# Kernel tuning notes

Hardware: AMD Instinct MI355X
Metric: run time of the kernel (lower is better)

The kernel has to match this reference:

```python
import jax, jax.numpy as jnp
import numpy as np

B, T, D, H, K = 8, 4096, 768, 12, 64
EPS_WKV = 1e-9
EPS_GN = 1e-5


def setup_inputs() -> dict:
    key = jax.random.key(0)
    ks = jax.random.split(key, 12)
    x = jax.random.normal(ks[0], (B, T, D), jnp.float32)
    # linear projection weights (torch nn.Linear stores [out, in]; y = x @ W.T)
    W_r = jax.random.normal(ks[1], (D, D), jnp.float32) * 0.02
    W_k = jax.random.normal(ks[2], (D, D), jnp.float32) * 0.02
    W_v = jax.random.normal(ks[3], (D, D), jnp.float32) * 0.02
    W_o = jax.random.normal(ks[4], (D, D), jnp.float32) * 0.02
    time_mix_r = jax.random.uniform(ks[5], (D,), jnp.float32)
    time_mix_k = jax.random.uniform(ks[6], (D,), jnp.float32)
    time_mix_v = jax.random.uniform(ks[7], (D,), jnp.float32)
    # around the module's init values (time_decay ~ -0.075, time_first ~ 0.15 at layer 6/12)
    time_decay = -0.075 + 0.1 * jax.random.normal(ks[8], (H, K), jnp.float32)
    time_first = 0.15 + 0.1 * jax.random.normal(ks[9], (H, K), jnp.float32)
    gn_weight = jnp.ones((D,), jnp.float32)
    gn_bias = jnp.zeros((D,), jnp.float32)
    return {
        "x": x,
        "time_mix_r": time_mix_r, "time_mix_k": time_mix_k, "time_mix_v": time_mix_v,
        "time_decay": time_decay, "time_first": time_first,
        "W_r": W_r, "W_k": W_k, "W_v": W_v, "W_o": W_o,
        "gn_weight": gn_weight, "gn_bias": gn_bias,
    }


def reference(x, time_mix_r, time_mix_k, time_mix_v, time_decay, time_first,
              W_r, W_k, W_v, W_o, gn_weight, gn_bias):
    Bx, Tx, Dx = x.shape
    Hx, Kx = time_decay.shape
    # token-shift: previous timestep (zero-initialized state)
    x_prev = jnp.concatenate([jnp.zeros_like(x[:, :1]), x[:, :-1]], axis=1)
    xr = x * time_mix_r + x_prev * (1.0 - time_mix_r)
    xk = x * time_mix_k + x_prev * (1.0 - time_mix_k)
    xv = x * time_mix_v + x_prev * (1.0 - time_mix_v)
    r = jax.nn.sigmoid(xr @ W_r.T).reshape(Bx, Tx, Hx, Kx)
    k = (xk @ W_k.T).reshape(Bx, Tx, Hx, Kx)
    v = (xv @ W_v.T).reshape(Bx, Tx, Hx, Kx)

    w = jnp.exp(-jnp.exp(time_decay))   # [H,K] decay per channel
    eu = jnp.exp(time_first)            # [H,K] bonus for current token

    def step(carry, kv_t):
        num, den = carry                # each [B,H,K]
        k_t, v_t = kv_t                 # each [B,H,K]
        ek = jnp.exp(k_t)
        wkv = (num + eu * ek * v_t) / (den + eu * ek + EPS_WKV)
        return (num * w + ek * v_t, den * w + ek), wkv

    k_tm = jnp.moveaxis(k, 1, 0)        # [T,B,H,K]
    v_tm = jnp.moveaxis(v, 1, 0)
    init = (jnp.zeros((Bx, Hx, Kx), x.dtype), jnp.zeros((Bx, Hx, Kx), x.dtype))
    _, wkv = jax.lax.scan(step, init, (k_tm, v_tm))
    out = jnp.moveaxis(wkv, 0, 1)       # [B,T,H,K]

    y = r * out                         # [B,T,H,K]
    # torch GroupNorm(H, D) on [B, D, T]: normalize each group over (K channels x T steps)
    mean = y.mean(axis=(1, 3), keepdims=True)
    var = y.var(axis=(1, 3), keepdims=True)
    y = (y - mean) * jax.lax.rsqrt(var + EPS_GN)
    y = y * gn_weight.reshape(1, 1, Hx, Kx) + gn_bias.reshape(1, 1, Hx, Kx)
    return y.reshape(Bx, Tx, Dx) @ W_o.T
```

## Files before the change

### kernel.cpp

```cpp
#include <hip/hip_runtime.h>
#include <hip/hip_bf16.h>
#include <cstdint>

#define B_ 8
#define T_ 4096
#define D_ 768
#define H_ 12
#define M_ (B_*T_)
#define CHUNKS 256
#define CLEN 16
#define WELEM (D_*D_)
#define NCH (B_*H_*64)

typedef __attribute__((ext_vector_type(8))) short bf16x8;
typedef __attribute__((ext_vector_type(4))) float f32x4;

static __device__ __forceinline__ unsigned short f2bf(float f) {
  __hip_bfloat16 h = __float2bfloat16(f);
  return __builtin_bit_cast(unsigned short, h);
}
static __device__ __forceinline__ float bf2f(unsigned short u) {
  unsigned v = ((unsigned)u) << 16;
  return __builtin_bit_cast(float, v);
}

static __device__ __forceinline__ void async16(const void* g, void* l) {
  __builtin_amdgcn_global_load_lds(
      (const __attribute__((address_space(1))) unsigned int*)g,
      (__attribute__((address_space(3))) unsigned int*)l, 16, 0, 0);
}

__global__ __launch_bounds__(256) void zero_out_kernel(float* __restrict__ out, size_t n4) {
  size_t gid = (size_t)blockIdx.x * 256 + threadIdx.x;
  if (gid < n4) *(float4*)(out + gid * 4) = make_float4(0.f, 0.f, 0.f, 0.f);
}

__global__ __launch_bounds__(256) void mix_kernel(
    const float* __restrict__ x, const float* __restrict__ tmr,
    const float* __restrict__ tmk, const float* __restrict__ tmv,
    unsigned short* __restrict__ xr, unsigned short* __restrict__ xk,
    unsigned short* __restrict__ xv) {
  size_t gid = (size_t)blockIdx.x * 256 + threadIdx.x;
  size_t idx4 = gid * 4;
  int d = (int)(idx4 % D_);
  size_t row = idx4 / D_;
  int t = (int)(row & (T_ - 1));
  float4 xc = *(const float4*)(x + idx4);
  float4 xp = make_float4(0.f, 0.f, 0.f, 0.f);
  if (t > 0) xp = *(const float4*)(x + idx4 - D_);
  float4 mr = *(const float4*)(tmr + d);
  float4 mk = *(const float4*)(tmk + d);
  float4 mv = *(const float4*)(tmv + d);
  ushort4 orr, okk, ovv;
  orr.x = f2bf(xc.x*mr.x + xp.x*(1.f-mr.x));
  orr.y = f2bf(xc.y*mr.y + xp.y*(1.f-mr.y));
  orr.z = f2bf(xc.z*mr.z + xp.z*(1.f-mr.z));
  orr.w = f2bf(xc.w*mr.w + xp.w*(1.f-mr.w));
  okk.x = f2bf(xc.x*mk.x + xp.x*(1.f-mk.x));
  okk.y = f2bf(xc.y*mk.y + xp.y*(1.f-mk.y));
  okk.z = f2bf(xc.z*mk.z + xp.z*(1.f-mk.z));
  okk.w = f2bf(xc.w*mk.w + xp.w*(1.f-mk.w));
  ovv.x = f2bf(xc.x*mv.x + xp.x*(1.f-mv.x));
  ovv.y = f2bf(xc.y*mv.y + xp.y*(1.f-mv.y));
  ovv.z = f2bf(xc.z*mv.z + xp.z*(1.f-mv.z));
  ovv.w = f2bf(xc.w*mv.w + xp.w*(1.f-mv.w));
  *(ushort4*)(xr + idx4) = orr;
  *(ushort4*)(xk + idx4) = okk;
  *(ushort4*)(xv + idx4) = ovv;
}

__global__ __launch_bounds__(256) void wconv_kernel(
    const float* __restrict__ a, const float* __restrict__ b,
    const float* __restrict__ c, const float* __restrict__ d,
    unsigned short* __restrict__ o) {
  size_t gid = (size_t)blockIdx.x * 256 + threadIdx.x;
  size_t idx4 = gid * 4;
  size_t mi = idx4 / WELEM;
  size_t off = idx4 % WELEM;
  const float* src = (mi == 0) ? a : (mi == 1) ? b : (mi == 2) ? c : d;
  float4 v = *(const float4*)(src + off);
  ushort4 u;
  u.x = f2bf(v.x); u.y = f2bf(v.y); u.z = f2bf(v.z); u.w = f2bf(v.w);
  *(ushort4*)(o + idx4) = u;
}

template<int ACT, int OBF>
__global__ __launch_bounds__(256) void gemm_nt(
    const unsigned short* __restrict__ A,
    const unsigned short* __restrict__ Bw,
    void* __restrict__ Cv, int M, int N, int Kd) {
  __shared__ __align__(16) unsigned short smem[4][128 * 64];
  const int tid = threadIdx.x;
  const int wave = tid >> 6, lane = tid & 63;
  const int quad = lane >> 4, l16 = lane & 15;

  int nwg = gridDim.x * gridDim.y;
  int lin = blockIdx.y * gridDim.x + blockIdx.x;
  int q = nwg >> 3, r = nwg & 7;
  int xcd = lin & 7, off = lin >> 3;
  int swz = (xcd < r ? xcd * (q + 1) : r * (q + 1) + (xcd - r) * q) + off;
  const int m0 = (swz / gridDim.x) * 128;
  const int n0 = (swz % gridDim.x) * 128;
  const int wm = (wave & 1) * 64, wn = (wave >> 1) * 64;

  auto stage = [&](int buf, int kb) {
    unsigned short* As = smem[buf];
    unsigned short* Bs = smem[buf] + 128 * 32;
#pragma unroll
    for (int j = 0; j < 2; ++j) {
      int chunk = j * 256 + tid;
      int row = chunk >> 2, slot = chunk & 3;
      int ks = slot ^ ((row >> 1) & 3);
      async16(A  + ((size_t)(m0 + row) * Kd + kb + ks * 8), &As[chunk * 8]);
      async16(Bw + ((size_t)(n0 + row) * Kd + kb + ks * 8), &Bs[chunk * 8]);
    }
  };

  f32x4 acc[4][4] = {};
  const int NT = Kd >> 5;

  stage(0, 0); stage(1, 32); stage(2, 64);
  for (int t = 0; t < NT; ++t) {
    if (t < NT - 2)       asm volatile("s_waitcnt vmcnt(8)" ::: "memory");
    else if (t == NT - 2) asm volatile("s_waitcnt vmcnt(4)" ::: "memory");
    else                  asm volatile("s_waitcnt vmcnt(0)" ::: "memory");
    __builtin_amdgcn_s_barrier();
    if (t + 3 < NT) stage((t + 3) & 3, (t + 3) * 32);
    const unsigned short* As = smem[t & 3];
    const unsigned short* Bs = smem[t & 3] + 128 * 32;
    bf16x8 a[4], b[4];
#pragma unroll
    for (int i = 0; i < 4; ++i) {
      int ra = wm + i * 16 + l16;
      a[i] = *(const bf16x8*)&As[ra * 32 + ((quad ^ ((ra >> 1) & 3)) * 8)];
      int rb = wn + i * 16 + l16;
      b[i] = *(const bf16x8*)&Bs[rb * 32 + ((quad ^ ((rb >> 1) & 3)) * 8)];
    }
#pragma unroll
    for (int i = 0; i < 4; ++i)
#pragma unroll
      for (int jj = 0; jj < 4; ++jj)
        acc[i][jj] = __builtin_amdgcn_mfma_f32_16x16x32_bf16(a[i], b[jj], acc[i][jj], 0, 0, 0);
  }

  if (OBF) {
    unsigned short* Cs = (unsigned short*)smem;
#pragma unroll
    for (int i = 0; i < 4; ++i) {
#pragma unroll
      for (int jj = 0; jj < 4; ++jj) {
        int col = wn + jj * 16 + l16;
#pragma unroll
        for (int rr = 0; rr < 4; ++rr) {
          int row = wm + i * 16 + quad * 4 + rr;
          float v = acc[i][jj][rr];
          if (ACT == 1) v = 1.f / (1.f + __expf(-v));
          int cg = (col >> 3) ^ (row & 7);
          Cs[row * 128 + cg * 8 + (col & 7)] = f2bf(v);
        }
      }
    }
    __syncthreads();
#pragma unroll
    for (int g = 0; g < 8; ++g) {
      int gi = g * 256 + tid;
      int row = gi >> 4, cg = gi & 15;
      int sg = cg ^ (row & 7);
      bf16x8 vv = *(const bf16x8*)&Cs[row * 128 + sg * 8];
      *(bf16x8*)((unsigned short*)Cv + (size_t)(m0 + row) * N + n0 + cg * 8) = vv;
    }
  } else {
#pragma unroll
    for (int i = 0; i < 4; ++i) {
      int rowb = m0 + wm + i * 16 + quad * 4;
#pragma unroll
      for (int jj = 0; jj < 4; ++jj) {
        int col = n0 + wn + jj * 16 + l16;
#pragma unroll
        for (int rr = 0; rr < 4; ++rr) {
          float v = acc[i][jj][rr];
          ((float*)Cv)[(size_t)(rowb + rr) * N + col] = v;
        }
      }
    }
  }
}

__global__ __launch_bounds__(256) void wkv_pass1(
    const unsigned short* __restrict__ Kb, const unsigned short* __restrict__ Vb,
    const float* __restrict__ td,
    float* __restrict__ sumN, float* __restrict__ sumD) {
  int gid = blockIdx.x * 256 + threadIdx.x;
  int kg = gid & 7;
  int tmp = gid >> 3;
  int h = tmp % H_;
  tmp /= H_;
  int b = tmp % B_;
  int c = tmp / B_;
  const float* tdp = td + h * 64 + kg * 8;
  float w[8], num[8], den[8];
#pragma unroll
  for (int j = 0; j < 8; ++j) {
    w[j] = __expf(-__expf(tdp[j]));
    num[j] = 0.f; den[j] = 0.f;
  }
  size_t base = ((size_t)(b * T_ + c * CLEN)) * D_ + h * 64 + kg * 8;
#pragma unroll 4
  for (int i = 0; i < CLEN; ++i) {
    bf16x8 k8 = *(const bf16x8*)(Kb + base + (size_t)i * D_);
    bf16x8 v8 = *(const bf16x8*)(Vb + base + (size_t)i * D_);
#pragma unroll
    for (int j = 0; j < 8; ++j) {
      float ek = __expf(bf2f((unsigned short)k8[j]));
      num[j] = num[j] * w[j] + ek * bf2f((unsigned short)v8[j]);
      den[j] = den[j] * w[j] + ek;
    }
  }
  int ob = ((c * B_ + b) * H_ + h) * 64 + kg * 8;
  *(float4*)(sumN + ob)     = make_float4(num[0], num[1], num[2], num[3]);
  *(float4*)(sumN + ob + 4) = make_float4(num[4], num[5], num[6], num[7]);
  *(float4*)(sumD + ob)     = make_float4(den[0], den[1], den[2], den[3]);
  *(float4*)(sumD + ob + 4) = make_float4(den[4], den[5], den[6], den[7]);
}

__global__ __launch_bounds__(256) void wkv_pass2(
    const float* __restrict__ sumN, const float* __restrict__ sumD,
    const float* __restrict__ td,
    float* __restrict__ prefN, float* __restrict__ prefD,
    float* __restrict__ gstats) {
  __shared__ float tile[256][64];
  int bid = blockIdx.x;
  if (bid == 0 && threadIdx.x < 192) gstats[threadIdx.x] = 0.f;
  int bh = bid >> 1, qd = bid & 1;
  const float* src = qd ? sumD : sumN;
  float* dst = qd ? prefD : prefN;
  int h = bh % H_;
  int base = bh * 64;
  int t = threadIdx.x;
  {
    int c4 = (t & 15) * 4;
    int rg = t >> 4;
#pragma unroll 4
    for (int i = 0; i < 16; ++i) {
      int row = rg * 16 + i;
      *(float4*)&tile[row][c4] = *(const float4*)&src[(size_t)row * NCH + base + c4];
    }
  }
  __syncthreads();
  int ch = t & 63, g = t >> 6;
  float w = __expf(-__expf(td[h * 64 + ch]));
  float wL = w;
#pragma unroll
  for (int i = 0; i < 4; ++i) wL *= wL;
  float v = 0.f;
  for (int i = 0; i < 64; ++i) {
    int row = g * 64 + i;
    v = v * wL + tile[row][ch];
    tile[row][ch] = v;
  }
  __syncthreads();
  float wL64 = wL;
#pragma unroll
  for (int i = 0; i < 6; ++i) wL64 *= wL64;
  float E = 0.f;
  for (int gp = 0; gp < g; ++gp)
    E = E * wL64 + tile[gp * 64 + 63][ch];
  float f = 1.f;
  for (int i = 0; i < 64; ++i) {
    int row = g * 64 + i;
    float P = (i == 0) ? E : tile[row - 1][ch] + E * f;
    dst[(size_t)row * NCH + base + ch] = P;
    f *= wL;
  }
}

__global__ __launch_bounds__(256) void wkv_pass3(
    const unsigned short* __restrict__ Kb, const unsigned short* __restrict__ Vb,
    unsigned short* __restrict__ RY,
    const float* __restrict__ td, const float* __restrict__ tf,
    const float* __restrict__ prefN, const float* __restrict__ prefD,
    float* __restrict__ gsum, float* __restrict__ gsq) {
  int gid = blockIdx.x * 256 + threadIdx.x;
  int kg = gid & 7;
  int tmp = gid >> 3;
  int h = tmp % H_;
  tmp /= H_;
  int b = tmp % B_;
  int c = tmp / B_;
  const float* tdp = td + h * 64 + kg * 8;
  const float* tfp = tf + h * 64 + kg * 8;
  float w[8], eu[8], num[8], den[8];
  int sb = ((c * B_ + b) * H_ + h) * 64 + kg * 8;
  float4 n0 = *(const float4*)(prefN + sb), n1 = *(const float4*)(prefN + sb + 4);
  float4 d0 = *(const float4*)(prefD + sb), d1 = *(const float4*)(prefD + sb + 4);
  num[0]=n0.x; num[1]=n0.y; num[2]=n0.z; num[3]=n0.w;
  num[4]=n1.x; num[5]=n1.y; num[6]=n1.z; num[7]=n1.w;
  den[0]=d0.x; den[1]=d0.y; den[2]=d0.z; den[3]=d0.w;
  den[4]=d1.x; den[5]=d1.y; den[6]=d1.z; den[7]=d1.w;
#pragma unroll
  for (int j = 0; j < 8; ++j) {
    w[j]  = __expf(-__expf(tdp[j]));
    eu[j] = __expf(tfp[j]);
  }
  size_t base = ((size_t)(b * T_ + c * CLEN)) * D_ + h * 64 + kg * 8;
  float s1 = 0.f, s2 = 0.f;
#pragma unroll 4
  for (int i = 0; i < CLEN; ++i) {
    size_t idx = base + (size_t)i * D_;
    bf16x8 k8 = *(const bf16x8*)(Kb + idx);
    bf16x8 v8 = *(const bf16x8*)(Vb + idx);
    bf16x8 r8 = *(const bf16x8*)(RY + idx);
    bf16x8 y8;
#pragma unroll
    for (int j = 0; j < 8; ++j) {
      float kk = bf2f((unsigned short)k8[j]);
      float vv = bf2f((unsigned short)v8[j]);
      float rr = bf2f((unsigned short)r8[j]);
      float ek = __expf(kk);
      float wkv = __fdividef(num[j] + eu[j] * ek * vv, den[j] + eu[j] * ek + 1e-9f);
      unsigned short ybf = f2bf(rr * wkv);
      y8[j] = (short)ybf;
      float y = bf2f(ybf);
      s1 += y; s2 += y * y;
      num[j] = num[j] * w[j] + ek * vv;
      den[j] = den[j] * w[j] + ek;
    }
    *(bf16x8*)(RY + idx) = y8;
  }
#pragma unroll
  for (int off = 4; off; off >>= 1) {
    s1 += __shfl_xor(s1, off);
    s2 += __shfl_xor(s2, off);
  }
  if (kg == 0) {
    atomicAdd(&gsum[b * H_ + h], s1);
    atomicAdd(&gsq [b * H_ + h], s2);
  }
}

__global__ __launch_bounds__(256) void gn_kernel(
    const unsigned short* __restrict__ Y, const float* __restrict__ gsum,
    const float* __restrict__ gsq, const float* __restrict__ gw,
    const float* __restrict__ gb, unsigned short* __restrict__ Ybf) {
  size_t gid = (size_t)blockIdx.x * 256 + threadIdx.x;
  size_t idx4 = gid * 4;
  int d = (int)(idx4 % D_);
  size_t row = idx4 / D_;
  int b = (int)(row >> 12);
  int h = d >> 6;
  int g = b * H_ + h;
  const float inv = 1.f / (float)(T_ * 64);
  float mean = gsum[g] * inv;
  float var = gsq[g] * inv - mean * mean;
  float rstd = rsqrtf(var + 1e-5f);
  ushort4 yu = *(const ushort4*)(Y + idx4);
  float4 wv = *(const float4*)(gw + d);
  float4 bv = *(const float4*)(gb + d);
  ushort4 o;
  o.x = f2bf((bf2f(yu.x) - mean) * rstd * wv.x + bv.x);
  o.y = f2bf((bf2f(yu.y) - mean) * rstd * wv.y + bv.y);
  o.z = f2bf((bf2f(yu.z) - mean) * rstd * wv.z + bv.z);
  o.w = f2bf((bf2f(yu.w) - mean) * rstd * wv.w + bv.w);
  *(ushort4*)(Ybf + idx4) = o;
}

extern "C" void kernel_launch(void* const* d_in, const int* in_sizes, int n_in,
                              void* d_out, int out_size, void* d_ws, size_t ws_size,
                              hipStream_t stream) {
  (void)in_sizes; (void)n_in;
  const float* x   = (const float*)d_in[0];
  const float* tmr = (const float*)d_in[1];
  const float* tmk = (const float*)d_in[2];
  const float* tmv = (const float*)d_in[3];
  const float* td  = (const float*)d_in[4];
  const float* tf  = (const float*)d_in[5];
  const float* Wr  = (const float*)d_in[6];
  const float* Wk  = (const float*)d_in[7];
  const float* Wv  = (const float*)d_in[8];
  const float* Wo  = (const float*)d_in[9];
  const float* gw  = (const float*)d_in[10];
  const float* gb  = (const float*)d_in[11];
  float* out = (float*)d_out;

  constexpr size_t MD = (size_t)M_ * D_;
  constexpr size_t NEED = 4 * (MD * 2)
                        + (size_t)4 * WELEM * 2
                        + 4 * ((size_t)CHUNKS * NCH * 4)
                        + 1024;
  if (ws_size < NEED) {
    zero_out_kernel<<<(int)((MD / 4 + 255) / 256), 256, 0, stream>>>(out, MD / 4);
    return;
  }

  char* ws = (char*)d_ws;
  unsigned short* XR = (unsigned short*)ws; ws += MD * 2;
  unsigned short* XK = (unsigned short*)ws; ws += MD * 2;
  unsigned short* XV = (unsigned short*)ws; ws += MD * 2;
  unsigned short* Rb = (unsigned short*)ws; ws += MD * 2;
  unsigned short* Wb = (unsigned short*)ws; ws += (size_t)4 * WELEM * 2;
  float* sumN  = (float*)ws; ws += (size_t)CHUNKS * NCH * 4;
  float* sumD  = (float*)ws; ws += (size_t)CHUNKS * NCH * 4;
  float* prefN = (float*)ws; ws += (size_t)CHUNKS * NCH * 4;
  float* prefD = (float*)ws; ws += (size_t)CHUNKS * NCH * 4;
  float* gstats = (float*)ws; ws += 1024;
  unsigned short* Kb = XR;
  unsigned short* Vb = XK;
  unsigned short* Yb = XV;

  mix_kernel<<<(int)(MD / 1024), 256, 0, stream>>>(x, tmr, tmk, tmv, XR, XK, XV);
  wconv_kernel<<<(4 * WELEM / 4) / 256, 256, 0, stream>>>(Wr, Wk, Wv, Wo, Wb);

  dim3 ggrid(D_ / 128, M_ / 128);
  gemm_nt<1, 1><<<ggrid, 256, 0, stream>>>(XR, Wb,             Rb, M_, D_, D_);
  gemm_nt<0, 1><<<ggrid, 256, 0, stream>>>(XK, Wb + WELEM,     Kb, M_, D_, D_);
  gemm_nt<0, 1><<<ggrid, 256, 0, stream>>>(XV, Wb + 2 * WELEM, Vb, M_, D_, D_);

  wkv_pass1<<<(CHUNKS * NCH / 8) / 256, 256, 0, stream>>>(Kb, Vb, td, sumN, sumD);
  wkv_pass2<<<192, 256, 0, stream>>>(sumN, sumD, td, prefN, prefD, gstats);
  wkv_pass3<<<(CHUNKS * NCH / 8) / 256, 256, 0, stream>>>(Kb, Vb, Rb, td, tf,
                                                          prefN, prefD, gstats, gstats + 96);
  gn_kernel<<<(int)(MD / 1024), 256, 0, stream>>>(Rb, gstats, gstats + 96, gw, gb, Yb);

  gemm_nt<0, 0><<<ggrid, 256, 0, stream>>>(Yb, Wb + 3 * WELEM, out, M_, D_, D_);
}
```

Measured before the change: 538.6 us.

## Fold GroupNorm into per-batch output weights and bias, drop gn pass

Result: faster. 515.8 us (-4.2%).

```diff
diff --git a/kernel.cpp b/kernel.cpp
--- a/kernel.cpp
+++ b/kernel.cpp
@@ -71,25 +71,24 @@
 
 __global__ __launch_bounds__(256) void wconv_kernel(
     const float* __restrict__ a, const float* __restrict__ b,
-    const float* __restrict__ c, const float* __restrict__ d,
-    unsigned short* __restrict__ o) {
+    const float* __restrict__ c, unsigned short* __restrict__ o) {
   size_t gid = (size_t)blockIdx.x * 256 + threadIdx.x;
   size_t idx4 = gid * 4;
   size_t mi = idx4 / WELEM;
   size_t off = idx4 % WELEM;
-  const float* src = (mi == 0) ? a : (mi == 1) ? b : (mi == 2) ? c : d;
+  const float* src = (mi == 0) ? a : (mi == 1) ? b : c;
   float4 v = *(const float4*)(src + off);
   ushort4 u;
   u.x = f2bf(v.x); u.y = f2bf(v.y); u.z = f2bf(v.z); u.w = f2bf(v.w);
   *(ushort4*)(o + idx4) = u;
 }
 
-template<int ACT, int OBF>
-__global__ __launch_bounds__(256) void gemm_nt(
+template<int ACT, int OBF, int BIAS>
+__global__ __launch_bounds__(256, 3) void gemm_nt(
     const unsigned short* __restrict__ A,
     const unsigned short* __restrict__ Bw,
-    void* __restrict__ Cv, int M, int N, int Kd) {
-  __shared__ __align__(16) unsigned short smem[4][128 * 64];
+    void* __restrict__ Cv, const float* __restrict__ bias2) {
+  __shared__ __align__(16) unsigned short smem[128 * 128];
   const int tid = threadIdx.x;
   const int wave = tid >> 6, lane = tid & 63;
   const int quad = lane >> 4, l16 = lane & 15;
@@ -102,32 +101,31 @@
   const int m0 = (swz / gridDim.x) * 128;
   const int n0 = (swz % gridDim.x) * 128;
   const int wm = (wave & 1) * 64, wn = (wave >> 1) * 64;
+  const int bb = m0 >> 12;
+  const unsigned short* Bp = BIAS ? Bw + (size_t)bb * WELEM : Bw;
 
   auto stage = [&](int buf, int kb) {
-    unsigned short* As = smem[buf];
-    unsigned short* Bs = smem[buf] + 128 * 32;
+    unsigned short* Ls = smem + buf * (128 * 64);
 #pragma unroll
     for (int j = 0; j < 2; ++j) {
       int chunk = j * 256 + tid;
       int row = chunk >> 2, slot = chunk & 3;
       int ks = slot ^ ((row >> 1) & 3);
-      async16(A  + ((size_t)(m0 + row) * Kd + kb + ks * 8), &As[chunk * 8]);
-      async16(Bw + ((size_t)(n0 + row) * Kd + kb + ks * 8), &Bs[chunk * 8]);
+      async16(A  + ((size_t)(m0 + row)) * D_ + kb + ks * 8, &Ls[chunk * 8]);
+      async16(Bp + ((size_t)(n0 + row)) * D_ + kb + ks * 8, &Ls[128 * 32 + chunk * 8]);
     }
   };
 
   f32x4 acc[4][4] = {};
-  const int NT = Kd >> 5;
-
-  stage(0, 0); stage(1, 32); stage(2, 64);
+  const int NT = D_ / 32;
+
+  stage(0, 0);
+  __syncthreads();
+  int cur = 0;
   for (int t = 0; t < NT; ++t) {
-    if (t < NT - 2)       asm volatile("s_waitcnt vmcnt(8)" ::: "memory");
-    else if (t == NT - 2) asm volatile("s_waitcnt vmcnt(4)" ::: "memory");
-    else                  asm volatile("s_waitcnt vmcnt(0)" ::: "memory");
-    __builtin_amdgcn_s_barrier();
-    if (t + 3 < NT) stage((t + 3) & 3, (t + 3) * 32);
-    const unsigned short* As = smem[t & 3];
-    const unsigned short* Bs = smem[t & 3] + 128 * 32;
+    if (t + 1 < NT) stage(cur ^ 1, (t + 1) * 32);
+    const unsigned short* As = smem + cur * (128 * 64);
+    const unsigned short* Bs = As + 128 * 32;
     bf16x8 a[4], b[4];
 #pragma unroll
     for (int i = 0; i < 4; ++i) {
@@ -141,10 +139,12 @@
 #pragma unroll
       for (int jj = 0; jj < 4; ++jj)
         acc[i][jj] = __builtin_amdgcn_mfma_f32_16x16x32_bf16(a[i], b[jj], acc[i][jj], 0, 0, 0);
+    __syncthreads();
+    cur ^= 1;
   }
 
   if (OBF) {
-    unsigned short* Cs = (unsigned short*)smem;
+    unsigned short* Cs = smem;
 #pragma unroll
     for (int i = 0; i < 4; ++i) {
 #pragma unroll
@@ -167,7 +167,7 @@
       int row = gi >> 4, cg = gi & 15;
       int sg = cg ^ (row & 7);
       bf16x8 vv = *(const bf16x8*)&Cs[row * 128 + sg * 8];
-      *(bf16x8*)((unsigned short*)Cv + (size_t)(m0 + row) * N + n0 + cg * 8) = vv;
+      *(bf16x8*)((unsigned short*)Cv + (size_t)(m0 + row) * D_ + n0 + cg * 8) = vv;
     }
   } else {
 #pragma unroll
@@ -176,10 +176,11 @@
 #pragma unroll
       for (int jj = 0; jj < 4; ++jj) {
         int col = n0 + wn + jj * 16 + l16;
+        float bias = BIAS ? bias2[bb * D_ + col] : 0.f;
 #pragma unroll
         for (int rr = 0; rr < 4; ++rr) {
-          float v = acc[i][jj][rr];
-          ((float*)Cv)[(size_t)(rowb + rr) * N + col] = v;
+          float v = acc[i][jj][rr] + bias;
+          ((float*)Cv)[(size_t)(rowb + rr) * D_ + col] = v;
         }
       }
     }
@@ -338,30 +339,56 @@
   }
 }
 
-__global__ __launch_bounds__(256) void gn_kernel(
-    const unsigned short* __restrict__ Y, const float* __restrict__ gsum,
+__global__ __launch_bounds__(256) void woprep_kernel(
+    const float* __restrict__ Wo, const float* __restrict__ gsum,
     const float* __restrict__ gsq, const float* __restrict__ gw,
-    const float* __restrict__ gb, unsigned short* __restrict__ Ybf) {
-  size_t gid = (size_t)blockIdx.x * 256 + threadIdx.x;
-  size_t idx4 = gid * 4;
-  int d = (int)(idx4 % D_);
-  size_t row = idx4 / D_;
-  int b = (int)(row >> 12);
-  int h = d >> 6;
-  int g = b * H_ + h;
+    unsigned short* __restrict__ Wob) {
+  int blk = blockIdx.x;
+  int b = blk / (WELEM / 1024);
+  size_t off = (size_t)(blk % (WELEM / 1024)) * 1024 + threadIdx.x * 4;
+  int d = (int)(off % D_);
+  int g = b * H_ + (d >> 6);
   const float inv = 1.f / (float)(T_ * 64);
   float mean = gsum[g] * inv;
   float var = gsq[g] * inv - mean * mean;
   float rstd = rsqrtf(var + 1e-5f);
-  ushort4 yu = *(const ushort4*)(Y + idx4);
-  float4 wv = *(const float4*)(gw + d);
-  float4 bv = *(const float4*)(gb + d);
+  float4 wo = *(const float4*)(Wo + off);
+  float4 gwv = *(const float4*)(gw + d);
   ushort4 o;
-  o.x = f2bf((bf2f(yu.x) - mean) * rstd * wv.x + bv.x);
-  o.y = f2bf((bf2f(yu.y) - mean) * rstd * wv.y + bv.y);
-  o.z = f2bf((bf2f(yu.z) - mean) * rstd * wv.z + bv.z);
-  o.w = f2bf((bf2f(yu.w) - mean) * rstd * wv.w + bv.w);
-  *(ushort4*)(Ybf + idx4) = o;
+  o.x = f2bf(wo.x * rstd * gwv.x);
+  o.y = f2bf(wo.y * rstd * gwv.y);
+  o.z = f2bf(wo.z * rstd * gwv.z);
+  o.w = f2bf(wo.w * rstd * gwv.w);
+  *(ushort4*)(Wob + (size_t)b * WELEM + off) = o;
+}
+
+__global__ __launch_bounds__(256) void bias2_kernel(
+    const float* __restrict__ Wo, const float* __restrict__ gsum,
+    const float* __restrict__ gsq, const float* __restrict__ gw,
+    const float* __restrict__ gb, float* __restrict__ bias2) {
+  int blk = blockIdx.x;
+  int b = blk / 12, nb = (blk % 12) * 64;
+  int lane = threadIdx.x & 63, wv = threadIdx.x >> 6;
+  const float inv = 1.f / (float)(T_ * 64);
+  float cB[12];
+#pragma unroll
+  for (int j = 0; j < 12; ++j) {
+    int d = lane + 64 * j;
+    int g = b * H_ + j;
+    float mean = gsum[g] * inv;
+    float var = gsq[g] * inv - mean * mean;
+    float rstd = rsqrtf(var + 1e-5f);
+    cB[j] = gb[d] - mean * rstd * gw[d];
+  }
+  for (int n = nb + wv * 16, e = n + 16; n < e; ++n) {
+    float s = 0.f;
+#pragma unroll
+    for (int j = 0; j < 12; ++j)
+      s += cB[j] * Wo[(size_t)n * D_ + lane + 64 * j];
+#pragma unroll
+    for (int off = 32; off; off >>= 1) s += __shfl_down(s, off);
+    if (lane == 0) bias2[b * D_ + n] = s;
+  }
 }
 
 extern "C" void kernel_launch(void* const* d_in, const int* in_sizes, int n_in,
@@ -405,21 +432,24 @@
   float* gstats = (float*)ws; ws += 1024;
   unsigned short* Kb = XR;
   unsigned short* Vb = XK;
-  unsigned short* Yb = XV;
+  unsigned short* Wob = (unsigned short*)sumN;
+  float* bias2 = prefN;
 
   mix_kernel<<<(int)(MD / 1024), 256, 0, stream>>>(x, tmr, tmk, tmv, XR, XK, XV);
-  wconv_kernel<<<(4 * WELEM / 4) / 256, 256, 0, stream>>>(Wr, Wk, Wv, Wo, Wb);
+  wconv_kernel<<<(3 * WELEM / 4) / 256, 256, 0, stream>>>(Wr, Wk, Wv, Wb);
 
   dim3 ggrid(D_ / 128, M_ / 128);
-  gemm_nt<1, 1><<<ggrid, 256, 0, stream>>>(XR, Wb,             Rb, M_, D_, D_);
-  gemm_nt<0, 1><<<ggrid, 256, 0, stream>>>(XK, Wb + WELEM,     Kb, M_, D_, D_);
-  gemm_nt<0, 1><<<ggrid, 256, 0, stream>>>(XV, Wb + 2 * WELEM, Vb, M_, D_, D_);
+  gemm_nt<1, 1, 0><<<ggrid, 256, 0, stream>>>(XR, Wb,             Rb, nullptr);
+  gemm_nt<0, 1, 0><<<ggrid, 256, 0, stream>>>(XK, Wb + WELEM,     Kb, nullptr);
+  gemm_nt<0, 1, 0><<<ggrid, 256, 0, stream>>>(XV, Wb + 2 * WELEM, Vb, nullptr);
 
   wkv_pass1<<<(CHUNKS * NCH / 8) / 256, 256, 0, stream>>>(Kb, Vb, td, sumN, sumD);
   wkv_pass2<<<192, 256, 0, stream>>>(sumN, sumD, td, prefN, prefD, gstats);
   wkv_pass3<<<(CHUNKS * NCH / 8) / 256, 256, 0, stream>>>(Kb, Vb, Rb, td, tf,
                                                           prefN, prefD, gstats, gstats + 96);
-  gn_kernel<<<(int)(MD / 1024), 256, 0, stream>>>(Rb, gstats, gstats + 96, gw, gb, Yb);
-
-  gemm_nt<0, 0><<<ggrid, 256, 0, stream>>>(Yb, Wb + 3 * WELEM, out, M_, D_, D_);
-}
+
+  woprep_kernel<<<8 * (WELEM / 1024), 256, 0, stream>>>(Wo, gstats, gstats + 96, gw, Wob);
+  bias2_kernel<<<96, 256, 0, stream>>>(Wo, gstats, gstats + 96, gw, gb, bias2);
+
+  gemm_nt<0, 0, 1><<<ggrid, 256, 0, stream>>>(Rb, Wob, out, bias2);
+}
```
